# Kernel optimization log

Hardware: AMD Instinct MI355X
Metric: run time of the kernel (lower is better)

## Reference

```python
import jax, jax.numpy as jnp
import numpy as np

B, J, D, H, W, AE, GH, NA, EH, L = 64, 20000, 32, 64, 4, 16, 24, 5000, 128, 32


def _ln(x, g=None, b=None, eps=1e-5):
    mu = x.mean(-1, keepdims=True)
    var = jnp.mean((x - mu) ** 2, axis=-1, keepdims=True)
    y = (x - mu) * jax.lax.rsqrt(var + eps)
    if g is not None:
        y = y * g + b
    return y


def setup_inputs():
    key = jax.random.key(0)
    ks = jax.random.split(key, 12)
    def rn(k, shape, s):
        return (jax.random.normal(k, shape) * s).astype(jnp.float32)
    return {
        "x": jax.random.normal(ks[0], (B, J), jnp.float32),
        "mask": jax.random.randint(ks[1], (B, J), 0, 2, jnp.int32),
        "atse_idx": jax.random.randint(ks[2], (J,), 0, NA, jnp.int32),
        "feature_embedding": jax.random.normal(ks[3], (J, D), jnp.float32),
        "atse_embedding": jax.random.normal(ks[4], (NA, AE), jnp.float32),
        "h_W1": rn(ks[5], (1 + D, H), 0.15), "h_b1": jnp.zeros((H,), jnp.float32),
        "h_ln1_g": jnp.ones((H,), jnp.float32), "h_ln1_b": jnp.zeros((H,), jnp.float32),
        "h_W2": rn(ks[6], (H, D), 0.12), "h_b2": jnp.zeros((D,), jnp.float32),
        "h_ln2_g": jnp.ones((D,), jnp.float32), "h_ln2_b": jnp.zeros((D,), jnp.float32),
        "g_W1": rn(ks[7], (D + AE, GH), 0.14), "g_b1": jnp.zeros((GH,), jnp.float32),
        "g_W2": rn(ks[8], (GH, W), 0.2), "g_b2": jnp.zeros((W,), jnp.float32),
        "c_W": rn(ks[9], (W * D, D), 0.09), "c_b": jnp.zeros((D,), jnp.float32),
        "c_ln_g": jnp.ones((D,), jnp.float32), "c_ln_b": jnp.zeros((D,), jnp.float32),
        "e_W1": rn(ks[10], (D, EH), 0.18), "e_b1": jnp.zeros((EH,), jnp.float32),
        "e_W2": rn(ks[11], (EH, 2 * L), 0.09), "e_b2": jnp.zeros((2 * L,), jnp.float32),
    }


def _forward(x, mask, atse_idx, feature_embedding, atse_embedding,
             h_W1, h_b1, h_ln1_g, h_ln1_b, h_W2, h_b2, h_ln2_g, h_ln2_b,
             g_W1, g_b1, g_W2, g_b2, c_W, c_b, c_ln_g, c_ln_b,
             e_W1, e_b1, e_W2, e_b2):
    TEMP = 1.0  # temperature_fixed=True -> scale = temperature_value
    Bv, Jv = x.shape
    Dv = feature_embedding.shape[1]
    # h-layer on all (b, j) pairs; LayerNorm/ReLU are per-row so this equals the
    # per-sample gather version on observed rows (unobserved rows get zero weight below).
    h_in = jnp.concatenate(
        [x[..., None], jnp.broadcast_to(feature_embedding[None], (Bv, Jv, Dv))], axis=-1)
    h = jax.nn.relu(_ln(h_in @ h_W1 + h_b1, h_ln1_g, h_ln1_b))
    h_out = jax.nn.relu(_ln(h @ h_W2 + h_b2, h_ln2_g, h_ln2_b))  # [B, J, D]
    # gate: [h_out | E_atse(j)] -> W head logits
    ae = atse_embedding[atse_idx]  # [J, AE]
    gate_in = jnp.concatenate(
        [h_out, jnp.broadcast_to(ae[None], (Bv, Jv, ae.shape[1]))], axis=-1)
    raw = jax.nn.relu(gate_in @ g_W1 + g_b1) @ g_W2 + g_b2  # [B, J, W]
    logits = jnp.clip(raw * TEMP, -10.0, 10.0)
    obs = mask.astype(bool)
    masked = jnp.where(obs[..., None], logits, -1e9)
    weights = jax.nn.softmax(masked, axis=1)  # softmax over observed junctions per head
    head_sums = jnp.einsum('bjw,bjd->bwd', weights, h_out)  # [B, W, D]
    Wn, Dn = head_sums.shape[1], head_sums.shape[2]
    combined = jax.nn.relu(_ln(head_sums.reshape(Bv, Wn * Dn) @ c_W + c_b, c_ln_g, c_ln_b))
    combined = jnp.where(obs.any(axis=1)[:, None], combined, 0.0)  # empty-mask rows -> zeros
    # encoder_mlp: scvi FCLayers, 2 layers, LayerNorm (no affine) + ReLU each
    e1 = jax.nn.relu(_ln(combined @ e_W1 + e_b1))
    mu_logvar = jax.nn.relu(_ln(e1 @ e_W2 + e_b2))
    mu, logvar = jnp.split(mu_logvar, 2, axis=-1)
    return mu, logvar


def reference(x, mask, atse_idx, feature_embedding, atse_embedding,
              h_W1, h_b1, h_ln1_g, h_ln1_b, h_W2, h_b2, h_ln2_g, h_ln2_b,
              g_W1, g_b1, g_W2, g_b2, c_W, c_b, c_ln_g, c_ln_b,
              e_W1, e_b1, e_W2, e_b2):
    return _forward(x, mask, atse_idx, feature_embedding, atse_embedding,
                    h_W1, h_b1, h_ln1_g, h_ln1_b, h_W2, h_b2, h_ln2_g, h_ln2_b,
                    g_W1, g_b1, g_W2, g_b2, c_W, c_b, c_ln_g, c_ln_b,
                    e_W1, e_b1, e_W2, e_b2)
```

## Files before the change

### kernel.cpp

```cpp
#include <hip/hip_runtime.h>
#include <hip/hip_bf16.h>
#include <math.h>

#define Bv 64
#define Jv 20000
#define NBT 8
#define NYB 125
#define ITERS 5

typedef __attribute__((ext_vector_type(8))) short short8;
typedef __attribute__((ext_vector_type(4))) float f32x4;

union U8 { short8 s; unsigned int u[4]; };

__device__ __forceinline__ unsigned short f2bf(float f) {
  unsigned int u = __float_as_uint(f);
  u += 0x7FFFu + ((u >> 16) & 1u);
  return (unsigned short)(u >> 16);
}
__device__ __forceinline__ unsigned int pkbf(float a, float b) {
  __hip_bfloat162 h = __float22bfloat162_rn(make_float2(a, b));
  union { __hip_bfloat162 h; unsigned int u; } c;
  c.h = h;
  return c.u;
}

__global__ __launch_bounds__(256) void pe_fused(
    const float* __restrict__ x, const int* __restrict__ mask,
    const int* __restrict__ atse_idx, const float* __restrict__ fe,
    const float* __restrict__ ae,
    const float* __restrict__ hW1, const float* __restrict__ hb1,
    const float* __restrict__ hl1g, const float* __restrict__ hl1b,
    const float* __restrict__ hW2, const float* __restrict__ hb2,
    const float* __restrict__ hl2g, const float* __restrict__ hl2b,
    const float* __restrict__ gW1, const float* __restrict__ gb1,
    const float* __restrict__ gW2, const float* __restrict__ gb2,
    float* __restrict__ acc_g, float* __restrict__ se_g) {
  __shared__ __align__(16) float s_pg[32 * 68];
  __shared__ __align__(16) float s_ex[32 * 4];
  __shared__ __align__(16) float s_gb[32 * 24 + 16];
  __shared__ __align__(16) float s_pair[256 * 4];
  __shared__ __align__(16) float s_w0[64], s_w0g[64], s_l1g[64], s_l1b[64];
  __shared__ __align__(16) float s_b2[32], s_l2g[32], s_l2b[32];
  __shared__ __align__(16) float s_gb1[24], s_gW2[96];
  __shared__ float s_gb2[4], s_scal[2];
  __shared__ __align__(16) float s_gW1bo[384];
  __shared__ unsigned char s_mk[256];
  __shared__ __align__(16) unsigned short s_gW1bf[32 * 24];
  __shared__ __align__(16) unsigned short s_ovl[256 * 34];

  int tid = threadIdx.x;
  int btile = blockIdx.x;
  int ytile = blockIdx.y;
  int lane = tid & 63, wv = tid >> 6;
  int li = lane & 15, quad = lane >> 4;
  unsigned short* s_h = s_ovl;

#define AEROW(j) ((float*)((char*)s_ovl + ((j) >> 3) * 4352 + 3712) + ((j) & 7) * 20)

  for (int i = tid; i < 768; i += 256) s_gW1bf[i] = f2bf(gW1[i]);
  for (int i = tid; i < 384; i += 256) s_gW1bo[i] = gW1[768 + i];
  if (tid < 96) s_gW2[tid] = gW2[tid];
  if (tid < 64) { s_w0[tid] = hW1[tid]; s_l1g[tid] = hl1g[tid]; s_l1b[tid] = hl1b[tid]; }
  if (tid < 32) { s_b2[tid] = hb2[tid]; s_l2g[tid] = hl2g[tid]; s_l2b[tid] = hl2b[tid]; }
  if (tid < 24) s_gb1[tid] = gb1[tid];
  if (tid < 4) s_gb2[tid] = gb2[tid];
  if (tid >= 224 && tid < 240) s_gb[32 * 24 + (tid - 224)] = 0.f;

  short8 bW2[2][2];
#pragma unroll
  for (int kt = 0; kt < 2; ++kt)
#pragma unroll
    for (int nt = 0; nt < 2; ++nt) {
      U8 t;
#pragma unroll
      for (int p = 0; p < 4; ++p) {
        float lo = hW2[(kt * 32 + quad * 8 + 2 * p) * 32 + nt * 16 + li];
        float hi = hW2[(kt * 32 + quad * 8 + 2 * p + 1) * 32 + nt * 16 + li];
        t.u[p] = pkbf(lo, hi);
      }
      bW2[kt][nt] = t.s;
    }
  U8 bH;
#pragma unroll
  for (int p = 0; p < 4; ++p) {
    float lo = hW1[(1 + quad * 8 + 2 * p) * 64 + wv * 16 + li];
    float hi = hW1[(1 + quad * 8 + 2 * p + 1) * 64 + wv * 16 + li];
    bH.u[p] = pkbf(lo, hi);
  }
  float hb = hb1[wv * 16 + li];

  __syncthreads();
  if (tid < 64) s_w0g[tid] = s_w0[tid] * s_l1g[tid];
  if (tid == 64) {
    float sw = 0.f, qw = 0.f;
    for (int k = 0; k < 64; ++k) { float w = s_w0[k]; sw += w; qw = fmaf(w, w, qw); }
    s_scal[0] = sw; s_scal[1] = qw;
  }

  f32x4 racc[2][2];
#pragma unroll
  for (int a = 0; a < 2; ++a)
#pragma unroll
    for (int c = 0; c < 2; ++c) {
      racc[a][c][0] = 0.f; racc[a][c][1] = 0.f; racc[a][c][2] = 0.f; racc[a][c][3] = 0.f;
    }
  float seacc[2] = {0.f, 0.f};

  int jp8 = tid >> 3, b8 = tid & 7;

  for (int it = 0; it < ITERS; ++it) {
    int J0 = (ytile * ITERS + it) * 32;

    if (tid < 32) {
      int ai = atse_idx[J0 + tid];
      const float4* av4 = (const float4*)(ae + (size_t)ai * 16);
      float* ar = AEROW(tid);
#pragma unroll
      for (int q = 0; q < 4; ++q) *(float4*)(ar + q * 4) = av4[q];
    }
    size_t xoff = (size_t)(btile * 8 + b8) * Jv + J0 + jp8;
    float xv = x[xoff];
    int mk = mask[xoff];
    {
      f32x4 cP;
#pragma unroll
      for (int mt = 0; mt < 2; ++mt) {
        cP[0] = hb; cP[1] = hb; cP[2] = hb; cP[3] = hb;
        const float* fp = fe + (size_t)(J0 + mt * 16 + li) * 32 + quad * 8;
        float4 f0 = *(const float4*)fp;
        float4 f1 = *(const float4*)(fp + 4);
        U8 aF;
        aF.u[0] = pkbf(f0.x, f0.y); aF.u[1] = pkbf(f0.z, f0.w);
        aF.u[2] = pkbf(f1.x, f1.y); aF.u[3] = pkbf(f1.z, f1.w);
        cP = __builtin_amdgcn_mfma_f32_16x16x32_bf16(aF.s, bH.s, cP, 0, 0, 0);
#pragma unroll
        for (int r = 0; r < 4; ++r)
          s_pg[(mt * 16 + quad * 4 + r) * 68 + wv * 16 + li] = cP[r];
      }
    }
    __syncthreads();

    {
      int c0 = b8 * 3;
      float g3[3] = {s_gb1[c0], s_gb1[c0 + 1], s_gb1[c0 + 2]};
      const float* ar = AEROW(jp8);
#pragma unroll 4
      for (int a = 0; a < 16; ++a) {
        float Av = ar[a];
        const float* gr = s_gW1bo + a * 24 + c0;
        g3[0] = fmaf(Av, gr[0], g3[0]);
        g3[1] = fmaf(Av, gr[1], g3[1]);
        g3[2] = fmaf(Av, gr[2], g3[2]);
      }
      s_gb[jp8 * 24 + c0] = g3[0];
      s_gb[jp8 * 24 + c0 + 1] = g3[1];
      s_gb[jp8 * 24 + c0 + 2] = g3[2];
    }
    {
      const float* pp = s_pg + jp8 * 68 + b8 * 8;
      float4 p0 = *(const float4*)pp, p1 = *(const float4*)(pp + 4);
      float4 wa = *(const float4*)(s_w0 + b8 * 8), wb = *(const float4*)(s_w0 + b8 * 8 + 4);
      float sp = p0.x + p0.y + p0.z + p0.w + p1.x + p1.y + p1.z + p1.w;
      float qp = fmaf(p0.x, p0.x, fmaf(p0.y, p0.y, fmaf(p0.z, p0.z, p0.w * p0.w)));
      qp = fmaf(p1.x, p1.x, fmaf(p1.y, p1.y, fmaf(p1.z, p1.z, fmaf(p1.w, p1.w, qp))));
      float dwp = fmaf(p0.x, wa.x, fmaf(p0.y, wa.y, fmaf(p0.z, wa.z, p0.w * wa.w)));
      dwp = fmaf(p1.x, wb.x, fmaf(p1.y, wb.y, fmaf(p1.z, wb.z, fmaf(p1.w, wb.w, dwp))));
#pragma unroll
      for (int off = 1; off < 8; off <<= 1) {
        sp += __shfl_xor(sp, off);
        qp += __shfl_xor(qp, off);
        dwp += __shfl_xor(dwp, off);
      }
      if (b8 == 0) ((float4*)s_ex)[jp8] = make_float4(sp, qp, dwp, 0.f);
    }
    {
      float4 exv = ((const float4*)s_ex)[jp8];
      float mu1 = fmaf(xv, s_scal[0], exv.x) * 0.015625f;
      float Et2 = fmaf(xv * xv, s_scal[1], fmaf(2.0f * xv, exv.z, exv.y)) * 0.015625f;
      float rs1 = rsqrtf(fmaxf(Et2 - mu1 * mu1, 0.f) + 1e-5f);
      *(float4*)(s_pair + tid * 4) = make_float4(xv * rs1, rs1, -mu1 * rs1, 0.f);
      s_mk[tid] = (unsigned char)mk;
    }

    {
      f32x4 cd[4][2];
      float b2a = s_b2[li], b2b = s_b2[16 + li];
#pragma unroll
      for (int t = 0; t < 4; ++t) {
        cd[t][0][0] = b2a; cd[t][0][1] = b2a; cd[t][0][2] = b2a; cd[t][0][3] = b2a;
        cd[t][1][0] = b2b; cd[t][1][1] = b2b; cd[t][1][2] = b2b; cd[t][1][3] = b2b;
      }
#pragma unroll
      for (int kt = 0; kt < 2; ++kt) {
        int base = kt * 32 + quad * 8;
        float4 wg0 = *(const float4*)(s_w0g + base);
        float4 wg1 = *(const float4*)(s_w0g + base + 4);
        float4 gg0 = *(const float4*)(s_l1g + base);
        float4 gg1 = *(const float4*)(s_l1g + base + 4);
        float4 bb0 = *(const float4*)(s_l1b + base);
        float4 bb1 = *(const float4*)(s_l1b + base + 4);
        float wg[8] = {wg0.x, wg0.y, wg0.z, wg0.w, wg1.x, wg1.y, wg1.z, wg1.w};
        float gg[8] = {gg0.x, gg0.y, gg0.z, gg0.w, gg1.x, gg1.y, gg1.z, gg1.w};
        float bb[8] = {bb0.x, bb0.y, bb0.z, bb0.w, bb1.x, bb1.y, bb1.z, bb1.w};
#pragma unroll
        for (int t = 0; t < 4; ++t) {
          int mrow = wv * 64 + t * 16 + li;
          float4 pr = *(const float4*)(s_pair + mrow * 4);
          const float* pgp = s_pg + (mrow >> 3) * 68 + base;
          float4 p0 = *(const float4*)pgp;
          float4 p1 = *(const float4*)(pgp + 4);
          float pv[8] = {p0.x, p0.y, p0.z, p0.w, p1.x, p1.y, p1.z, p1.w};
          float av[8];
#pragma unroll
          for (int i = 0; i < 8; ++i)
            av[i] = fmaxf(fmaf(fmaf(pr.y, pv[i], pr.z), gg[i], fmaf(pr.x, wg[i], bb[i])), 0.f);
          U8 a8;
          a8.u[0] = pkbf(av[0], av[1]); a8.u[1] = pkbf(av[2], av[3]);
          a8.u[2] = pkbf(av[4], av[5]); a8.u[3] = pkbf(av[6], av[7]);
          cd[t][0] = __builtin_amdgcn_mfma_f32_16x16x32_bf16(a8.s, bW2[kt][0], cd[t][0], 0, 0, 0);
          cd[t][1] = __builtin_amdgcn_mfma_f32_16x16x32_bf16(a8.s, bW2[kt][1], cd[t][1], 0, 0, 0);
        }
      }
      float g0 = s_l2g[li], be0 = s_l2b[li];
      float g1v = s_l2g[16 + li], be1 = s_l2b[16 + li];
#pragma unroll
      for (int t = 0; t < 4; ++t) {
        float sum[4], sq[4];
#pragma unroll
        for (int r = 0; r < 4; ++r) {
          float a = cd[t][0][r], b = cd[t][1][r];
          sum[r] = a + b;
          sq[r] = fmaf(a, a, b * b);
        }
#pragma unroll
        for (int off = 1; off < 16; off <<= 1) {
#pragma unroll
          for (int r = 0; r < 4; ++r) {
            sum[r] += __shfl_xor(sum[r], off);
            sq[r] += __shfl_xor(sq[r], off);
          }
        }
#pragma unroll
        for (int r = 0; r < 4; ++r) {
          float mu = sum[r] * 0.03125f;
          float var = sq[r] * 0.03125f - mu * mu;
          float rs2 = rsqrtf(fmaxf(var, 0.f) + 1e-5f);
          int m = wv * 64 + t * 16 + quad * 4 + r;
          float h0 = fmaxf(fmaf((cd[t][0][r] - mu) * rs2, g0, be0), 0.f);
          float h1 = fmaxf(fmaf((cd[t][1][r] - mu) * rs2, g1v, be1), 0.f);
          s_h[m * 34 + li] = f2bf(h0);
          s_h[m * 34 + 16 + li] = f2bf(h1);
        }
      }
    }

    {
      short8 aG0, aG1;
#pragma unroll
      for (int i = 0; i < 8; ++i) {
        int k = quad * 8 + i;
        aG0[i] = (short)s_gW1bf[k * 24 + li];
        aG1[i] = (li < 8) ? (short)s_gW1bf[k * 24 + 16 + li] : (short)0;
      }
      float4 gw4[2][4];
#pragma unroll
      for (int mt = 0; mt < 2; ++mt)
#pragma unroll
        for (int r = 0; r < 4; ++r) {
          int c = mt * 16 + quad * 4 + r;
          gw4[mt][r] = (c < 24) ? ((const float4*)s_gW2)[c]
                                : make_float4(0.f, 0.f, 0.f, 0.f);
        }
#pragma unroll
      for (int nt = 0; nt < 4; ++nt) {
        int m = wv * 64 + nt * 16 + li;
        U8 bu;
        const unsigned short* hp = s_h + m * 34 + quad * 8;
        bu.u[0] = *(const unsigned int*)(hp + 0);
        bu.u[1] = *(const unsigned int*)(hp + 2);
        bu.u[2] = *(const unsigned int*)(hp + 4);
        bu.u[3] = *(const unsigned int*)(hp + 6);
        int j = m >> 3;
        f32x4 c0, c1;
#pragma unroll
        for (int r = 0; r < 4; ++r) {
          c0[r] = s_gb[j * 24 + quad * 4 + r];
          c1[r] = s_gb[j * 24 + 16 + quad * 4 + r];
        }
        c0 = __builtin_amdgcn_mfma_f32_16x16x32_bf16(aG0, bu.s, c0, 0, 0, 0);
        c1 = __builtin_amdgcn_mfma_f32_16x16x32_bf16(aG1, bu.s, c1, 0, 0, 0);
        float r0 = s_gb2[0], r1 = s_gb2[1], r2 = s_gb2[2], r3 = s_gb2[3];
#pragma unroll
        for (int r = 0; r < 4; ++r) {
          float v0 = fmaxf(c0[r], 0.f);
          float v1 = fmaxf(c1[r], 0.f);
          float4 ga = gw4[0][r], gb = gw4[1][r];
          r0 = fmaf(v0, ga.x, fmaf(v1, gb.x, r0));
          r1 = fmaf(v0, ga.y, fmaf(v1, gb.y, r1));
          r2 = fmaf(v0, ga.z, fmaf(v1, gb.z, r2));
          r3 = fmaf(v0, ga.w, fmaf(v1, gb.w, r3));
        }
        r0 += __shfl_xor(r0, 16); r0 += __shfl_xor(r0, 32);
        r1 += __shfl_xor(r1, 16); r1 += __shfl_xor(r1, 32);
        r2 += __shfl_xor(r2, 16); r2 += __shfl_xor(r2, 32);
        r3 += __shfl_xor(r3, 16); r3 += __shfl_xor(r3, 32);
        r0 = fminf(fmaxf(r0, -10.f), 10.f);
        r1 = fminf(fmaxf(r1, -10.f), 10.f);
        r2 = fminf(fmaxf(r2, -10.f), 10.f);
        r3 = fminf(fmaxf(r3, -10.f), 10.f);
        bool act = (s_mk[m] != 0);
        float e0 = act ? __expf(r0 - 10.f) : 0.f;
        float e1 = act ? __expf(r1 - 10.f) : 0.f;
        float e2 = act ? __expf(r2 - 10.f) : 0.f;
        float e3 = act ? __expf(r3 - 10.f) : 0.f;
        if (quad == 0) *(float4*)(s_pair + m * 4) = make_float4(e0, e1, e2, e3);
      }
    }
    __syncthreads();

    {
      const float* s_e2 = s_pair;
#pragma unroll
      for (int bs = 0; bs < 2; ++bs) {
        int b = wv * 2 + bs;
        float ev[8];
        float sep = 0.f;
#pragma unroll
        for (int i = 0; i < 8; ++i) {
          float v = s_e2[((quad * 8 + i) * 8 + b) * 4 + (li & 3)];
          v = (li < 4) ? v : 0.f;
          ev[i] = v;
          sep += v;
        }
        seacc[bs] += sep;
        U8 a8;
        a8.u[0] = pkbf(ev[0], ev[1]); a8.u[1] = pkbf(ev[2], ev[3]);
        a8.u[2] = pkbf(ev[4], ev[5]); a8.u[3] = pkbf(ev[6], ev[7]);
#pragma unroll
        for (int half = 0; half < 2; ++half) {
          U8 bh;
#pragma unroll
          for (int p = 0; p < 4; ++p) {
            unsigned int lo = s_h[((quad * 8 + 2 * p) * 8 + b) * 34 + half * 16 + li];
            unsigned int hi = s_h[((quad * 8 + 2 * p + 1) * 8 + b) * 34 + half * 16 + li];
            bh.u[p] = lo | (hi << 16);
          }
          racc[bs][half] = __builtin_amdgcn_mfma_f32_16x16x32_bf16(a8.s, bh.s, racc[bs][half], 0, 0, 0);
        }
      }
    }
    __syncthreads();
  }

#pragma unroll
  for (int bs = 0; bs < 2; ++bs) {
    float se = seacc[bs];
    se += __shfl_xor(se, 16);
    se += __shfl_xor(se, 32);
    if (quad == 0) {
      int bg = btile * 8 + wv * 2 + bs;
      float* dst = acc_g + (size_t)bg * 128;
#pragma unroll
      for (int half = 0; half < 2; ++half)
#pragma unroll
        for (int r = 0; r < 4; ++r)
          atomicAdd(dst + r * 32 + half * 16 + li, racc[bs][half][r]);
      if (li < 4) atomicAdd(&se_g[bg * 4 + li], se);
    }
  }
#undef AEROW
}

__global__ __launch_bounds__(64) void pe_tail(
    const float* __restrict__ acc_g, const float* __restrict__ se_g,
    const float* __restrict__ cW, const float* __restrict__ cb,
    const float* __restrict__ clng, const float* __restrict__ clnb,
    const float* __restrict__ eW1, const float* __restrict__ eb1,
    const float* __restrict__ eW2, const float* __restrict__ eb2,
    float* __restrict__ out) {
  int b = blockIdx.x;
  int lane = threadIdx.x;
  __shared__ float s_hs[128], s_comb[32], s_e1[128];

  float se0 = se_g[b * 4 + 0];
  bool empty = !(se0 > 0.0f);
  float inv[4];
#pragma unroll
  for (int w = 0; w < 4; ++w) {
    float sw = se_g[b * 4 + w];
    inv[w] = empty ? 0.0f : 1.0f / sw;
  }
  s_hs[lane] = acc_g[b * 128 + lane] * inv[lane >> 5];
  s_hs[lane + 64] = acc_g[b * 128 + lane + 64] * inv[(lane + 64) >> 5];
  __syncthreads();

  if (lane < 32) {
    float cp = cb[lane];
#pragma unroll 8
    for (int i = 0; i < 128; ++i) cp = fmaf(s_hs[i], cW[i * 32 + lane], cp);
    float ssum = cp;
#pragma unroll
    for (int off = 16; off > 0; off >>= 1) ssum += __shfl_xor(ssum, off, 32);
    float mu = ssum * (1.0f / 32.0f);
    float dd = cp - mu;
    float sq = dd * dd;
#pragma unroll
    for (int off = 16; off > 0; off >>= 1) sq += __shfl_xor(sq, off, 32);
    float rs = rsqrtf(sq * (1.0f / 32.0f) + 1e-5f);
    float comb = fmaxf(fmaf(dd * rs, clng[lane], clnb[lane]), 0.0f);
    if (empty) comb = 0.0f;
    s_comb[lane] = comb;
  }
  __syncthreads();

  float v0 = eb1[lane], v1 = eb1[lane + 64];
#pragma unroll
  for (int i = 0; i < 32; ++i) {
    float c = s_comb[i];
    v0 = fmaf(c, eW1[i * 128 + lane], v0);
    v1 = fmaf(c, eW1[i * 128 + lane + 64], v1);
  }
  float ssum = v0 + v1;
#pragma unroll
  for (int off = 32; off > 0; off >>= 1) ssum += __shfl_xor(ssum, off, 64);
  float mu = ssum * (1.0f / 128.0f);
  float d0 = v0 - mu, d1 = v1 - mu;
  float sq = fmaf(d0, d0, d1 * d1);
#pragma unroll
  for (int off = 32; off > 0; off >>= 1) sq += __shfl_xor(sq, off, 64);
  float rs = rsqrtf(sq * (1.0f / 128.0f) + 1e-5f);
  s_e1[lane] = fmaxf(d0 * rs, 0.0f);
  s_e1[lane + 64] = fmaxf(d1 * rs, 0.0f);
  __syncthreads();

  float v = eb2[lane];
#pragma unroll 8
  for (int i = 0; i < 128; ++i) v = fmaf(s_e1[i], eW2[i * 64 + lane], v);
  ssum = v;
#pragma unroll
  for (int off = 32; off > 0; off >>= 1) ssum += __shfl_xor(ssum, off, 64);
  mu = ssum * (1.0f / 64.0f);
  float dv = v - mu;
  sq = dv * dv;
#pragma unroll
  for (int off = 32; off > 0; off >>= 1) sq += __shfl_xor(sq, off, 64);
  rs = rsqrtf(sq * (1.0f / 64.0f) + 1e-5f);
  float o = fmaxf(dv * rs, 0.0f);
  if (lane < 32)
    out[b * 32 + lane] = o;
  else
    out[Bv * 32 + b * 32 + (lane - 32)] = o;
}

extern "C" void kernel_launch(void* const* d_in, const int* in_sizes, int n_in,
                              void* d_out, int out_size, void* d_ws, size_t ws_size,
                              hipStream_t stream) {
  const float* x    = (const float*)d_in[0];
  const int* mask   = (const int*)d_in[1];
  const int* atse   = (const int*)d_in[2];
  const float* fe   = (const float*)d_in[3];
  const float* ae   = (const float*)d_in[4];
  const float* hW1  = (const float*)d_in[5];
  const float* hb1  = (const float*)d_in[6];
  const float* hl1g = (const float*)d_in[7];
  const float* hl1b = (const float*)d_in[8];
  const float* hW2  = (const float*)d_in[9];
  const float* hb2  = (const float*)d_in[10];
  const float* hl2g = (const float*)d_in[11];
  const float* hl2b = (const float*)d_in[12];
  const float* gW1  = (const float*)d_in[13];
  const float* gb1  = (const float*)d_in[14];
  const float* gW2  = (const float*)d_in[15];
  const float* gb2  = (const float*)d_in[16];
  const float* cW   = (const float*)d_in[17];
  const float* cb   = (const float*)d_in[18];
  const float* clng = (const float*)d_in[19];
  const float* clnb = (const float*)d_in[20];
  const float* eW1  = (const float*)d_in[21];
  const float* eb1  = (const float*)d_in[22];
  const float* eW2  = (const float*)d_in[23];
  const float* eb2  = (const float*)d_in[24];
  float* out = (float*)d_out;

  float* ws = (float*)d_ws;
  float* accg = ws;
  float* seg  = accg + Bv * 128;

  hipMemsetAsync(accg, 0, (Bv * 128 + Bv * 4) * sizeof(float), stream);

  pe_fused<<<dim3(NBT, NYB), dim3(256), 0, stream>>>(
      x, mask, atse, fe, ae, hW1, hb1, hl1g, hl1b, hW2, hb2, hl2g, hl2b,
      gW1, gb1, gW2, gb2, accg, seg);
  pe_tail<<<dim3(Bv), dim3(64), 0, stream>>>(
      accg, seg, cW, cb, clng, clnb, eW1, eb1, eW2, eb2, out);
}
```

Before: 226.7 us.

## Replace shuffles with DPP/permlane reductions, pad LDS rows, hoist gate weights

Cross-lane reductions that used __shfl_xor (which goes through ds_bpermute) now use DPP row operations and permlane16/32 swap instructions. The padded LDS row stride for the h tile grows from 34 to 36 so rows can be read with 8-byte loads, and the AE gate weights are stored transposed so the projection can use float4 vector loads. The gate A-fragments are built once outside the loop instead of every iteration, s_ex is folded into spare s_pg padding, and launch bounds now request 4 blocks per CU. The intent is fewer LDS instructions and less reduction latency. In exchange the kernel depends on gfx950-specific inline asm and carries more live registers.

New measurement: 288.4 us. 27.2% more time.

```diff
diff --git a/kernel.cpp b/kernel.cpp
--- a/kernel.cpp
+++ b/kernel.cpp
@@ -10,6 +10,7 @@
 
 typedef __attribute__((ext_vector_type(8))) short short8;
 typedef __attribute__((ext_vector_type(4))) float f32x4;
+typedef __attribute__((ext_vector_type(2))) unsigned int u32x2;
 
 union U8 { short8 s; unsigned int u[4]; };
 
@@ -25,7 +26,23 @@
   return c.u;
 }
 
-__global__ __launch_bounds__(256) void pe_fused(
+template <int CTRL>
+__device__ __forceinline__ float dppadd(float v) {
+  int t = __builtin_amdgcn_update_dpp(0, __float_as_int(v), CTRL, 0xF, 0xF, true);
+  return v + __int_as_float(t);
+}
+__device__ __forceinline__ float pl16sum(float v) {
+  float a = v, b = v;
+  asm("v_permlane16_swap_b32 %0, %1" : "+v"(a), "+v"(b));
+  return a + b;
+}
+__device__ __forceinline__ float pl32sum(float v) {
+  float a = v, b = v;
+  asm("v_permlane32_swap_b32 %0, %1" : "+v"(a), "+v"(b));
+  return a + b;
+}
+
+__global__ __launch_bounds__(256, 4) void pe_fused(
     const float* __restrict__ x, const int* __restrict__ mask,
     const int* __restrict__ atse_idx, const float* __restrict__ fe,
     const float* __restrict__ ae,
@@ -37,17 +54,16 @@
     const float* __restrict__ gW2, const float* __restrict__ gb2,
     float* __restrict__ acc_g, float* __restrict__ se_g) {
   __shared__ __align__(16) float s_pg[32 * 68];
-  __shared__ __align__(16) float s_ex[32 * 4];
   __shared__ __align__(16) float s_gb[32 * 24 + 16];
   __shared__ __align__(16) float s_pair[256 * 4];
   __shared__ __align__(16) float s_w0[64], s_w0g[64], s_l1g[64], s_l1b[64];
   __shared__ __align__(16) float s_b2[32], s_l2g[32], s_l2b[32];
   __shared__ __align__(16) float s_gb1[24], s_gW2[96];
   __shared__ float s_gb2[4], s_scal[2];
-  __shared__ __align__(16) float s_gW1bo[384];
+  __shared__ __align__(16) float s_gW1aT[24 * 16];
   __shared__ unsigned char s_mk[256];
   __shared__ __align__(16) unsigned short s_gW1bf[32 * 24];
-  __shared__ __align__(16) unsigned short s_ovl[256 * 34];
+  __shared__ __align__(16) unsigned short s_ovl[256 * 36];
 
   int tid = threadIdx.x;
   int btile = blockIdx.x;
@@ -56,10 +72,11 @@
   int li = lane & 15, quad = lane >> 4;
   unsigned short* s_h = s_ovl;
 
-#define AEROW(j) ((float*)((char*)s_ovl + ((j) >> 3) * 4352 + 3712) + ((j) & 7) * 20)
+#define AEROW(j) ((float*)((char*)s_ovl + ((j) >> 3) * 4608 + 3968) + ((j) & 7) * 20)
 
   for (int i = tid; i < 768; i += 256) s_gW1bf[i] = f2bf(gW1[i]);
-  for (int i = tid; i < 384; i += 256) s_gW1bo[i] = gW1[768 + i];
+  for (int i = tid; i < 384; i += 256)
+    s_gW1aT[i] = gW1[768 + (i & 15) * 24 + (i >> 4)];
   if (tid < 96) s_gW2[tid] = gW2[tid];
   if (tid < 64) { s_w0[tid] = hW1[tid]; s_l1g[tid] = hl1g[tid]; s_l1b[tid] = hl1b[tid]; }
   if (tid < 32) { s_b2[tid] = hb2[tid]; s_l2g[tid] = hl2g[tid]; s_l2b[tid] = hl2b[tid]; }
@@ -96,6 +113,13 @@
     float sw = 0.f, qw = 0.f;
     for (int k = 0; k < 64; ++k) { float w = s_w0[k]; sw += w; qw = fmaf(w, w, qw); }
     s_scal[0] = sw; s_scal[1] = qw;
+  }
+  short8 aG0, aG1;
+#pragma unroll
+  for (int i = 0; i < 8; ++i) {
+    int k = quad * 8 + i;
+    aG0[i] = (short)s_gW1bf[k * 24 + li];
+    aG1[i] = (li < 8) ? (short)s_gW1bf[k * 24 + 16 + li] : (short)0;
   }
 
   f32x4 racc[2][2];
@@ -143,19 +167,20 @@
 
     {
       int c0 = b8 * 3;
-      float g3[3] = {s_gb1[c0], s_gb1[c0 + 1], s_gb1[c0 + 2]};
       const float* ar = AEROW(jp8);
-#pragma unroll 4
-      for (int a = 0; a < 16; ++a) {
-        float Av = ar[a];
-        const float* gr = s_gW1bo + a * 24 + c0;
-        g3[0] = fmaf(Av, gr[0], g3[0]);
-        g3[1] = fmaf(Av, gr[1], g3[1]);
-        g3[2] = fmaf(Av, gr[2], g3[2]);
-      }
-      s_gb[jp8 * 24 + c0] = g3[0];
-      s_gb[jp8 * 24 + c0 + 1] = g3[1];
-      s_gb[jp8 * 24 + c0 + 2] = g3[2];
+      float4 A0 = *(const float4*)ar, A1 = *(const float4*)(ar + 4);
+      float4 A2 = *(const float4*)(ar + 8), A3 = *(const float4*)(ar + 12);
+#pragma unroll
+      for (int c = 0; c < 3; ++c) {
+        const float4* tr = (const float4*)(s_gW1aT + (c0 + c) * 16);
+        float4 t0 = tr[0], t1 = tr[1], t2 = tr[2], t3 = tr[3];
+        float g = s_gb1[c0 + c];
+        g = fmaf(A0.x, t0.x, fmaf(A0.y, t0.y, fmaf(A0.z, t0.z, fmaf(A0.w, t0.w, g))));
+        g = fmaf(A1.x, t1.x, fmaf(A1.y, t1.y, fmaf(A1.z, t1.z, fmaf(A1.w, t1.w, g))));
+        g = fmaf(A2.x, t2.x, fmaf(A2.y, t2.y, fmaf(A2.z, t2.z, fmaf(A2.w, t2.w, g))));
+        g = fmaf(A3.x, t3.x, fmaf(A3.y, t3.y, fmaf(A3.z, t3.z, fmaf(A3.w, t3.w, g))));
+        s_gb[jp8 * 24 + c0 + c] = g;
+      }
     }
     {
       const float* pp = s_pg + jp8 * 68 + b8 * 8;
@@ -166,16 +191,13 @@
       qp = fmaf(p1.x, p1.x, fmaf(p1.y, p1.y, fmaf(p1.z, p1.z, fmaf(p1.w, p1.w, qp))));
       float dwp = fmaf(p0.x, wa.x, fmaf(p0.y, wa.y, fmaf(p0.z, wa.z, p0.w * wa.w)));
       dwp = fmaf(p1.x, wb.x, fmaf(p1.y, wb.y, fmaf(p1.z, wb.z, fmaf(p1.w, wb.w, dwp))));
-#pragma unroll
-      for (int off = 1; off < 8; off <<= 1) {
-        sp += __shfl_xor(sp, off);
-        qp += __shfl_xor(qp, off);
-        dwp += __shfl_xor(dwp, off);
-      }
-      if (b8 == 0) ((float4*)s_ex)[jp8] = make_float4(sp, qp, dwp, 0.f);
-    }
-    {
-      float4 exv = ((const float4*)s_ex)[jp8];
+      sp = dppadd<0xB1>(sp); sp = dppadd<0x4E>(sp); sp = dppadd<0x141>(sp);
+      qp = dppadd<0xB1>(qp); qp = dppadd<0x4E>(qp); qp = dppadd<0x141>(qp);
+      dwp = dppadd<0xB1>(dwp); dwp = dppadd<0x4E>(dwp); dwp = dppadd<0x141>(dwp);
+      if (b8 == 0) *(float4*)(s_pg + jp8 * 68 + 64) = make_float4(sp, qp, dwp, 0.f);
+    }
+    {
+      float4 exv = *(const float4*)(s_pg + jp8 * 68 + 64);
       float mu1 = fmaf(xv, s_scal[0], exv.x) * 0.015625f;
       float Et2 = fmaf(xv * xv, s_scal[1], fmaf(2.0f * xv, exv.z, exv.y)) * 0.015625f;
       float rs1 = rsqrtf(fmaxf(Et2 - mu1 * mu1, 0.f) + 1e-5f);
@@ -234,12 +256,11 @@
           sq[r] = fmaf(a, a, b * b);
         }
 #pragma unroll
-        for (int off = 1; off < 16; off <<= 1) {
-#pragma unroll
-          for (int r = 0; r < 4; ++r) {
-            sum[r] += __shfl_xor(sum[r], off);
-            sq[r] += __shfl_xor(sq[r], off);
-          }
+        for (int r = 0; r < 4; ++r) {
+          sum[r] = dppadd<0xB1>(sum[r]); sum[r] = dppadd<0x4E>(sum[r]);
+          sum[r] = dppadd<0x124>(sum[r]); sum[r] = dppadd<0x128>(sum[r]);
+          sq[r] = dppadd<0xB1>(sq[r]); sq[r] = dppadd<0x4E>(sq[r]);
+          sq[r] = dppadd<0x124>(sq[r]); sq[r] = dppadd<0x128>(sq[r]);
         }
 #pragma unroll
         for (int r = 0; r < 4; ++r) {
@@ -249,20 +270,13 @@
           int m = wv * 64 + t * 16 + quad * 4 + r;
           float h0 = fmaxf(fmaf((cd[t][0][r] - mu) * rs2, g0, be0), 0.f);
           float h1 = fmaxf(fmaf((cd[t][1][r] - mu) * rs2, g1v, be1), 0.f);
-          s_h[m * 34 + li] = f2bf(h0);
-          s_h[m * 34 + 16 + li] = f2bf(h1);
-        }
-      }
-    }
-
-    {
-      short8 aG0, aG1;
-#pragma unroll
-      for (int i = 0; i < 8; ++i) {
-        int k = quad * 8 + i;
-        aG0[i] = (short)s_gW1bf[k * 24 + li];
-        aG1[i] = (li < 8) ? (short)s_gW1bf[k * 24 + 16 + li] : (short)0;
-      }
+          s_h[m * 36 + li] = f2bf(h0);
+          s_h[m * 36 + 16 + li] = f2bf(h1);
+        }
+      }
+    }
+
+    {
       float4 gw4[2][4];
 #pragma unroll
       for (int mt = 0; mt < 2; ++mt)
@@ -276,11 +290,9 @@
       for (int nt = 0; nt < 4; ++nt) {
         int m = wv * 64 + nt * 16 + li;
         U8 bu;
-        const unsigned short* hp = s_h + m * 34 + quad * 8;
-        bu.u[0] = *(const unsigned int*)(hp + 0);
-        bu.u[1] = *(const unsigned int*)(hp + 2);
-        bu.u[2] = *(const unsigned int*)(hp + 4);
-        bu.u[3] = *(const unsigned int*)(hp + 6);
+        const u32x2* hp2 = (const u32x2*)(s_h + m * 36 + quad * 8);
+        u32x2 h01 = hp2[0], h23 = hp2[1];
+        bu.u[0] = h01[0]; bu.u[1] = h01[1]; bu.u[2] = h23[0]; bu.u[3] = h23[1];
         int j = m >> 3;
         f32x4 c0, c1;
 #pragma unroll
@@ -301,10 +313,10 @@
           r2 = fmaf(v0, ga.z, fmaf(v1, gb.z, r2));
           r3 = fmaf(v0, ga.w, fmaf(v1, gb.w, r3));
         }
-        r0 += __shfl_xor(r0, 16); r0 += __shfl_xor(r0, 32);
-        r1 += __shfl_xor(r1, 16); r1 += __shfl_xor(r1, 32);
-        r2 += __shfl_xor(r2, 16); r2 += __shfl_xor(r2, 32);
-        r3 += __shfl_xor(r3, 16); r3 += __shfl_xor(r3, 32);
+        r0 = pl32sum(pl16sum(r0));
+        r1 = pl32sum(pl16sum(r1));
+        r2 = pl32sum(pl16sum(r2));
+        r3 = pl32sum(pl16sum(r3));
         r0 = fminf(fmaxf(r0, -10.f), 10.f);
         r1 = fminf(fmaxf(r1, -10.f), 10.f);
         r2 = fminf(fmaxf(r2, -10.f), 10.f);
@@ -342,8 +354,8 @@
           U8 bh;
 #pragma unroll
           for (int p = 0; p < 4; ++p) {
-            unsigned int lo = s_h[((quad * 8 + 2 * p) * 8 + b) * 34 + half * 16 + li];
-            unsigned int hi = s_h[((quad * 8 + 2 * p + 1) * 8 + b) * 34 + half * 16 + li];
+            unsigned int lo = s_h[((quad * 8 + 2 * p) * 8 + b) * 36 + half * 16 + li];
+            unsigned int hi = s_h[((quad * 8 + 2 * p + 1) * 8 + b) * 36 + half * 16 + li];
             bh.u[p] = lo | (hi << 16);
           }
           racc[bs][half] = __builtin_amdgcn_mfma_f32_16x16x32_bf16(a8.s, bh.s, racc[bs][half], 0, 0, 0);
@@ -356,8 +368,7 @@
 #pragma unroll
   for (int bs = 0; bs < 2; ++bs) {
     float se = seacc[bs];
-    se += __shfl_xor(se, 16);
-    se += __shfl_xor(se, 32);
+    se = pl32sum(pl16sum(se));
     if (quad == 0) {
       int bg = btile * 8 + wv * 2 + bs;
       float* dst = acc_g + (size_t)bg * 128;
```
